# Kernel optimization log

Measured on AMD Instinct MI355X. Metric: run time of the kernel, lower is better.

The kernel has to match this reference:

```python
import jax, jax.numpy as jnp
import numpy as np
import math

# tcnn HashGrid config (hard-coded in the torch module)
N_LEVELS = 16
N_FEATS = 2
LOG2_T = 19
T = 1 << LOG2_T            # 524288 entries per level
BASE_RES = 16
PER_LEVEL_SCALE = 1.4472692012786865
PRIMES = (1, 2654435761, 805459861)  # tcnn coherent spatial hash primes
N_POINTS = 1 << 20

# 8 trilinear corner offsets, [8, 3]
_OFFSETS = np.stack(np.meshgrid(*([np.arange(2)] * 3), indexing='ij'), -1).reshape(8, 3)


def _level_scale_res(level):
    # tcnn: grid_scale = base * s^l - 1 ; resolution = ceil(grid_scale) + 1
    scale = BASE_RES * (PER_LEVEL_SCALE ** level) - 1.0
    res = int(math.ceil(scale)) + 1
    return scale, res


def hashgrid_encode(coords, table):
    """coords: [..., 3] in [0,1]; table: [N_LEVELS, T, N_FEATS].
    Returns [..., N_LEVELS * N_FEATS]."""
    lead_shape = coords.shape[:-1]
    x = coords.reshape(-1, 3)                         # [N, 3]
    offs_i = jnp.asarray(_OFFSETS, dtype=jnp.uint32)  # [8, 3]
    offs_f = jnp.asarray(_OFFSETS, dtype=coords.dtype)
    feats = []
    for l in range(N_LEVELS):
        scale, res = _level_scale_res(l)
        pos = x * jnp.asarray(scale, x.dtype) + 0.5   # [N, 3]
        pf = jnp.floor(pos)
        w = pos - pf                                   # trilinear weights in [0,1)
        grid = pf.astype(jnp.uint32)                  # [N, 3]
        c = grid[None, :, :] + offs_i[:, None, :]     # [8, N, 3] corner coords
        if res ** 3 <= T:
            # dense (non-hashed) indexing for coarse levels
            cc = jnp.minimum(c, jnp.uint32(res - 1)).astype(jnp.int32)
            idx = cc[..., 0] + cc[..., 1] * res + cc[..., 2] * (res * res)
        else:
            # spatial hash: XOR of per-dim prime products, mod 2^19
            h = (c[..., 0] * jnp.uint32(PRIMES[0])
                 ^ c[..., 1] * jnp.uint32(PRIMES[1])
                 ^ c[..., 2] * jnp.uint32(PRIMES[2]))
            idx = (h & jnp.uint32(T - 1)).astype(jnp.int32)
        v = table[l][idx]                             # [8, N, F] gathered features
        # per-corner trilinear weight: prod over dims of (w or 1-w)
        wc = jnp.prod(jnp.where(offs_f[:, None, :] == 1.0, w[None], 1.0 - w[None]), axis=-1)  # [8, N]
        feats.append(jnp.einsum('kn,knf->nf', wc, v))  # [N, F]
    out = jnp.concatenate(feats, axis=-1)             # [N, 32]
    return out.reshape(*lead_shape, N_LEVELS * N_FEATS)


def setup_inputs() -> dict:
    key = jax.random.key(0)
    k1, k2 = jax.random.split(key)
    coords = jax.random.uniform(k1, (N_POINTS, 3), dtype=jnp.float32)
    # tcnn initializes hash table uniform in [-1e-4, 1e-4]
    table = jax.random.uniform(k2, (N_LEVELS, T, N_FEATS), dtype=jnp.float32,
                               minval=-1e-4, maxval=1e-4)
    return {"coords": coords, "table": table}


def reference(coords, table):
    return hashgrid_encode(coords, table)
```

## Files before the change

kernel.cpp:

```cpp
#include <hip/hip_runtime.h>
#include <math.h>

#define TBL   (1u << 19)
#define TMASK (TBL - 1u)
#define PRIME1 2654435761u
#define PRIME2 805459861u

typedef float v2f __attribute__((ext_vector_type(2)));

struct LevelParams {
    float    scale[16];
    unsigned res[16];
    unsigned dense[16];
};

__device__ __forceinline__ void corner_indices(
    float x, float y, float z, float s, unsigned res, unsigned dense,
    unsigned idx[8], float* wx, float* wy, float* wz)
{
    float px = __fadd_rn(__fmul_rn(x, s), 0.5f);
    float py = __fadd_rn(__fmul_rn(y, s), 0.5f);
    float pz = __fadd_rn(__fmul_rn(z, s), 0.5f);
    float fx = floorf(px), fy = floorf(py), fz = floorf(pz);
    *wx = px - fx; *wy = py - fy; *wz = pz - fz;
    unsigned gx = (unsigned)fx, gy = (unsigned)fy, gz = (unsigned)fz;

    if (dense) {
        const unsigned rm1 = res - 1u;
        unsigned cx0 = min(gx, rm1),   cx1 = min(gx + 1u, rm1);
        unsigned cy0 = min(gy, rm1),   cy1 = min(gy + 1u, rm1);
        unsigned cz0 = min(gz, rm1),   cz1 = min(gz + 1u, rm1);
        unsigned y0 = cy0 * res,       y1 = cy1 * res;
        unsigned z0 = cz0 * res * res, z1 = cz1 * res * res;
        idx[0] = cx0 + y0 + z0;  idx[1] = cx0 + y0 + z1;
        idx[2] = cx0 + y1 + z0;  idx[3] = cx0 + y1 + z1;
        idx[4] = cx1 + y0 + z0;  idx[5] = cx1 + y0 + z1;
        idx[6] = cx1 + y1 + z0;  idx[7] = cx1 + y1 + z1;
    } else {
        unsigned hx0 = gx,          hx1 = gx + 1u;
        unsigned hy0 = gy * PRIME1, hy1 = hy0 + PRIME1;
        unsigned hz0 = gz * PRIME2, hz1 = hz0 + PRIME2;
        idx[0] = (hx0 ^ hy0 ^ hz0) & TMASK;
        idx[1] = (hx0 ^ hy0 ^ hz1) & TMASK;
        idx[2] = (hx0 ^ hy1 ^ hz0) & TMASK;
        idx[3] = (hx0 ^ hy1 ^ hz1) & TMASK;
        idx[4] = (hx1 ^ hy0 ^ hz0) & TMASK;
        idx[5] = (hx1 ^ hy0 ^ hz1) & TMASK;
        idx[6] = (hx1 ^ hy1 ^ hz0) & TMASK;
        idx[7] = (hx1 ^ hy1 ^ hz1) & TMASK;
    }
}

__device__ __forceinline__ v2f interp_level(
    const float2* __restrict__ tab,
    float x, float y, float z, float s, unsigned res, unsigned dense)
{
    unsigned idx[8];
    float wx, wy, wz;
    corner_indices(x, y, z, s, res, dense, idx, &wx, &wy, &wz);

    float2 v[8];
    #pragma unroll
    for (int k = 0; k < 8; ++k) v[k] = tab[idx[k]];

    float wx0 = 1.f - wx, wy0 = 1.f - wy, wz0 = 1.f - wz;
    float wyz00 = wy0 * wz0, wyz01 = wy0 * wz;
    float wyz10 = wy  * wz0, wyz11 = wy  * wz;
    float cw[8] = { wx0 * wyz00, wx0 * wyz01, wx0 * wyz10, wx0 * wyz11,
                    wx  * wyz00, wx  * wyz01, wx  * wyz10, wx  * wyz11 };

    float f0 = 0.f, f1 = 0.f;
    #pragma unroll
    for (int k = 0; k < 8; ++k) {
        f0 = fmaf(cw[k], v[k].x, f0);
        f1 = fmaf(cw[k], v[k].y, f1);
    }
    v2f r; r.x = f0; r.y = f1;
    return r;
}

__global__ __launch_bounds__(256, 8) void pass_a(
    const float* __restrict__ coords,
    const float* __restrict__ table,
    v2f* __restrict__ ws,
    LevelParams lp, unsigned n)
{
    const unsigned l = blockIdx.y;
    const unsigned p = blockIdx.x * 256u + threadIdx.x;
    if (p >= n) return;

    const float x = coords[3ull * p + 0];
    const float y = coords[3ull * p + 1];
    const float z = coords[3ull * p + 2];

    const float2* __restrict__ tab = (const float2*)table + (size_t)l * TBL;
    v2f r = interp_level(tab, x, y, z, lp.scale[l], lp.res[l], lp.dense[l]);
    __builtin_nontemporal_store(r, ws + (size_t)l * n + p);
}

__global__ __launch_bounds__(256, 4) void pass_b(
    const v2f* __restrict__ ws,
    float* __restrict__ out, unsigned n)
{
    __shared__ float lds[256 * 33];
    const unsigned t  = threadIdx.x;
    const unsigned p0 = blockIdx.x * 256u;
    const unsigned p  = p0 + t;

    #pragma unroll
    for (int l = 0; l < 16; ++l) {
        v2f v = {0.f, 0.f};
        if (p < n) v = __builtin_nontemporal_load(ws + (size_t)l * n + p);
        lds[t * 33u + 2u * l]      = v.x;
        lds[t * 33u + 2u * l + 1u] = v.y;
    }
    __syncthreads();

    const size_t base  = (size_t)p0 * 32u;
    const size_t total = (size_t)n * 32u;
    #pragma unroll
    for (int i = 0; i < 32; ++i) {
        size_t j = (size_t)i * 256u + t;
        size_t o = base + j;
        if (o < total)
            __builtin_nontemporal_store(
                lds[(unsigned)(j >> 5) * 33u + ((unsigned)j & 31u)], out + o);
    }
}

__global__ __launch_bounds__(256, 4) void hashgrid_enc(
    const float* __restrict__ coords,
    const float* __restrict__ table,
    float* __restrict__ out,
    LevelParams lp, unsigned n)
{
    __shared__ float lds[256 * 33];
    const unsigned t = threadIdx.x;
    const unsigned p = blockIdx.x * 256u + t;

    float x = 0.f, y = 0.f, z = 0.f;
    if (p < n) {
        x = coords[3ull * p + 0];
        y = coords[3ull * p + 1];
        z = coords[3ull * p + 2];
    }

    #pragma unroll 2
    for (int l = 0; l < 16; ++l) {
        const float2* __restrict__ tab = (const float2*)table + (size_t)l * TBL;
        v2f r = interp_level(tab, x, y, z, lp.scale[l], lp.res[l], lp.dense[l]);
        lds[t * 33u + 2u * l]      = r.x;
        lds[t * 33u + 2u * l + 1u] = r.y;
    }
    __syncthreads();

    const size_t base  = (size_t)blockIdx.x * 8192u;
    const size_t total = (size_t)n * 32u;
    #pragma unroll
    for (int i = 0; i < 32; ++i) {
        size_t j = (size_t)i * 256u + t;
        size_t o = base + j;
        if (o < total)
            out[o] = lds[(unsigned)(j >> 5) * 33u + ((unsigned)j & 31u)];
    }
}

extern "C" void kernel_launch(void* const* d_in, const int* in_sizes, int n_in,
                              void* d_out, int out_size, void* d_ws, size_t ws_size,
                              hipStream_t stream) {
    (void)n_in; (void)out_size;
    const float* coords = (const float*)d_in[0];
    const float* table  = (const float*)d_in[1];
    float* out = (float*)d_out;

    LevelParams lp;
    for (int l = 0; l < 16; ++l) {
        double scale = 16.0 * pow(1.4472692012786865, (double)l) - 1.0;
        int res = (int)ceil(scale) + 1;
        lp.scale[l] = (float)scale;
        lp.res[l]   = (unsigned)res;
        long long r3 = (long long)res * res * res;
        lp.dense[l] = (r3 <= (long long)TBL) ? 1u : 0u;
    }

    unsigned n = (unsigned)(in_sizes[0] / 3);
    unsigned chunks = (n + 255u) / 256u;
    size_t ws_needed = (size_t)16 * n * sizeof(v2f);

    if (ws_size >= ws_needed) {
        v2f* ws = (v2f*)d_ws;
        hipLaunchKernelGGL(pass_a, dim3(chunks, 16), dim3(256), 0, stream,
                           coords, table, ws, lp, n);
        hipLaunchKernelGGL(pass_b, dim3(chunks), dim3(256), 0, stream,
                           ws, out, n);
    } else {
        hipLaunchKernelGGL(hashgrid_enc, dim3(chunks), dim3(256), 0, stream,
                           coords, table, out, lp, n);
    }
}
```

Before: 720.6 us.

## Gather table pairs as 16-byte loads and simplify transpose pass to direct vector stores

Each corner lookup now reads an aligned 16-byte chunk holding two adjacent table entries and selects the right half by index parity, instead of an 8-byte float2 load. This keeps gather requests aligned to wider units, but each lookup moves twice the bytes, which could raise pressure on the cache hierarchy. The second pass drops its LDS transpose and barrier: each thread reads its 16 per-level pairs and writes 32 contiguous floats as eight 16-byte stores. Those stores are strided across threads rather than coalesced, and the nontemporal hints on the workspace loads and output stores are removed.

```diff
diff --git a/kernel.cpp b/kernel.cpp
--- a/kernel.cpp
+++ b/kernel.cpp
@@ -7,6 +7,7 @@
 #define PRIME2 805459861u
 
 typedef float v2f __attribute__((ext_vector_type(2)));
+typedef float v4f __attribute__((ext_vector_type(4)));
 
 struct LevelParams {
     float    scale[16];
@@ -52,28 +53,33 @@
 }
 
 __device__ __forceinline__ v2f interp_level(
-    const float2* __restrict__ tab,
+    const v4f* __restrict__ tab4,
     float x, float y, float z, float s, unsigned res, unsigned dense)
 {
     unsigned idx[8];
     float wx, wy, wz;
     corner_indices(x, y, z, s, res, dense, idx, &wx, &wy, &wz);
 
-    float2 v[8];
-    #pragma unroll
-    for (int k = 0; k < 8; ++k) v[k] = tab[idx[k]];
-
     float wx0 = 1.f - wx, wy0 = 1.f - wy, wz0 = 1.f - wz;
     float wyz00 = wy0 * wz0, wyz01 = wy0 * wz;
     float wyz10 = wy  * wz0, wyz11 = wy  * wz;
-    float cw[8] = { wx0 * wyz00, wx0 * wyz01, wx0 * wyz10, wx0 * wyz11,
-                    wx  * wyz00, wx  * wyz01, wx  * wyz10, wx  * wyz11 };
+    float cw0[4] = { wx0 * wyz00, wx0 * wyz01, wx0 * wyz10, wx0 * wyz11 };
+    float cw1[4] = { wx  * wyz00, wx  * wyz01, wx  * wyz10, wx  * wyz11 };
 
     float f0 = 0.f, f1 = 0.f;
     #pragma unroll
-    for (int k = 0; k < 8; ++k) {
-        f0 = fmaf(cw[k], v[k].x, f0);
-        f1 = fmaf(cw[k], v[k].y, f1);
+    for (int k = 0; k < 4; ++k) {
+        unsigned i0 = idx[k], i1 = idx[k + 4];
+        v4f q0 = tab4[i0 >> 1];
+        v4f q1 = tab4[i1 >> 1];
+        float a0 = (i0 & 1u) ? q0.z : q0.x;
+        float b0 = (i0 & 1u) ? q0.w : q0.y;
+        float a1 = (i1 & 1u) ? q1.z : q1.x;
+        float b1 = (i1 & 1u) ? q1.w : q1.y;
+        f0 = fmaf(cw0[k], a0, f0);
+        f1 = fmaf(cw0[k], b0, f1);
+        f0 = fmaf(cw1[k], a1, f0);
+        f1 = fmaf(cw1[k], b1, f1);
     }
     v2f r; r.x = f0; r.y = f1;
     return r;
@@ -93,38 +99,30 @@
     const float y = coords[3ull * p + 1];
     const float z = coords[3ull * p + 2];
 
-    const float2* __restrict__ tab = (const float2*)table + (size_t)l * TBL;
-    v2f r = interp_level(tab, x, y, z, lp.scale[l], lp.res[l], lp.dense[l]);
+    const v4f* __restrict__ tab4 = (const v4f*)(table + (size_t)l * (2u * TBL));
+    v2f r = interp_level(tab4, x, y, z, lp.scale[l], lp.res[l], lp.dense[l]);
     __builtin_nontemporal_store(r, ws + (size_t)l * n + p);
 }
 
-__global__ __launch_bounds__(256, 4) void pass_b(
+__global__ __launch_bounds__(256, 8) void pass_b(
     const v2f* __restrict__ ws,
     float* __restrict__ out, unsigned n)
 {
-    __shared__ float lds[256 * 33];
-    const unsigned t  = threadIdx.x;
-    const unsigned p0 = blockIdx.x * 256u;
-    const unsigned p  = p0 + t;
+    const unsigned p = blockIdx.x * 256u + threadIdx.x;
+    if (p >= n) return;
 
+    v2f v[16];
     #pragma unroll
-    for (int l = 0; l < 16; ++l) {
-        v2f v = {0.f, 0.f};
-        if (p < n) v = __builtin_nontemporal_load(ws + (size_t)l * n + p);
-        lds[t * 33u + 2u * l]      = v.x;
-        lds[t * 33u + 2u * l + 1u] = v.y;
-    }
-    __syncthreads();
+    for (int l = 0; l < 16; ++l)
+        v[l] = ws[(size_t)l * n + p];
 
-    const size_t base  = (size_t)p0 * 32u;
-    const size_t total = (size_t)n * 32u;
+    v4f* __restrict__ out4 = (v4f*)out;
     #pragma unroll
-    for (int i = 0; i < 32; ++i) {
-        size_t j = (size_t)i * 256u + t;
-        size_t o = base + j;
-        if (o < total)
-            __builtin_nontemporal_store(
-                lds[(unsigned)(j >> 5) * 33u + ((unsigned)j & 31u)], out + o);
+    for (int i = 0; i < 8; ++i) {
+        v4f o;
+        o.x = v[2 * i].x;     o.y = v[2 * i].y;
+        o.z = v[2 * i + 1].x; o.w = v[2 * i + 1].y;
+        out4[(size_t)p * 8u + i] = o;
     }
 }
 
@@ -147,8 +145,8 @@
 
     #pragma unroll 2
     for (int l = 0; l < 16; ++l) {
-        const float2* __restrict__ tab = (const float2*)table + (size_t)l * TBL;
-        v2f r = interp_level(tab, x, y, z, lp.scale[l], lp.res[l], lp.dense[l]);
+        const v4f* __restrict__ tab4 = (const v4f*)(table + (size_t)l * (2u * TBL));
+        v2f r = interp_level(tab4, x, y, z, lp.scale[l], lp.res[l], lp.dense[l]);
         lds[t * 33u + 2u * l]      = r.x;
         lds[t * 33u + 2u * l + 1u] = r.y;
     }
```

After: 691.9 us. 1.04x faster.
